# Kernel tuning notes

Hardware: AMD Instinct MI355X
Metric: run time of the kernel (lower is better)

The kernel has to match this reference:

```python
import jax, jax.numpy as jnp
import numpy as np

EMBED = 512
HEADS = 8
HEAD_DIM = EMBED // HEADS
LN_EPS = 1e-5


def setup_inputs() -> dict:
    key = jax.random.key(0)
    ks = jax.random.split(key, 13)
    B, L = 4, 2048
    s = 1.0 / np.sqrt(EMBED)
    inp = {
        "values": jax.random.normal(ks[0], (B, L, EMBED), dtype=jnp.float32),
        "keys": jax.random.normal(ks[1], (B, L, EMBED), dtype=jnp.float32),
        "query": jax.random.normal(ks[2], (B, L, EMBED), dtype=jnp.float32),
        "Wq": jax.random.uniform(ks[3], (EMBED, EMBED), jnp.float32, -s, s),
        "bq": jax.random.uniform(ks[4], (EMBED,), jnp.float32, -s, s),
        "Wk": jax.random.uniform(ks[5], (EMBED, EMBED), jnp.float32, -s, s),
        "bk": jax.random.uniform(ks[6], (EMBED,), jnp.float32, -s, s),
        "Wv": jax.random.uniform(ks[7], (EMBED, EMBED), jnp.float32, -s, s),
        "bv": jax.random.uniform(ks[8], (EMBED,), jnp.float32, -s, s),
        "Wo": jax.random.uniform(ks[9], (EMBED, EMBED), jnp.float32, -s, s),
        "bo": jax.random.uniform(ks[10], (EMBED,), jnp.float32, -s, s),
        "ln_g": jnp.ones((EMBED,), jnp.float32),
        "ln_b": jnp.zeros((EMBED,), jnp.float32),
    }
    return inp


def reference(values, keys, query, Wq, bq, Wk, bk, Wv, bv, Wo, bo, ln_g, ln_b):
    B, L, _ = query.shape
    # separate QKV linears (torch Linear: x @ W^T + b)
    Q = (query @ Wq.T + bq).reshape(B, L, HEADS, HEAD_DIM)
    K = (keys @ Wk.T + bk).reshape(B, L, HEADS, HEAD_DIM)
    V = (values @ Wv.T + bv).reshape(B, L, HEADS, HEAD_DIM)
    # explicit QK^T scores: [B, H, Q, K]
    scores = jnp.einsum("nqhd,nkhd->nhqk", Q, K) / np.sqrt(HEAD_DIM)
    attn = jax.nn.softmax(scores, axis=-1)
    out = jnp.einsum("nhqk,nkhd->nqhd", attn, V).reshape(B, L, EMBED)
    out = out @ Wo.T + bo
    # residual + LayerNorm (dropout = identity in eval)
    x = out + query
    mu = jnp.mean(x, axis=-1, keepdims=True)
    var = jnp.var(x, axis=-1, keepdims=True)
    return (x - mu) * jax.lax.rsqrt(var + LN_EPS) * ln_g + ln_b
```

## Files before the change

### kernel.cpp

```cpp
#include <hip/hip_runtime.h>

typedef short bf16x8 __attribute__((ext_vector_type(8)));
typedef short s16x4 __attribute__((ext_vector_type(4)));
typedef float f32x4 __attribute__((ext_vector_type(4)));
typedef unsigned int uint4v __attribute__((ext_vector_type(4)));
typedef unsigned int uint2v __attribute__((ext_vector_type(2)));

#define BLM   8192
#define EMB   512
#define LSEQ  2048
#define NHEAD 8
#define HDIM  64

typedef __attribute__((address_space(3))) char lds_ch;

__device__ __forceinline__ unsigned short f2bf(float x) {
    unsigned int u = __builtin_bit_cast(unsigned int, x);
    u += 0x7FFFu + ((u >> 16) & 1u);
    return (unsigned short)(u >> 16);
}

__device__ __forceinline__ unsigned int cvtpk(float lo, float hi) {
    unsigned int r;
    asm("v_cvt_pk_bf16_f32 %0, %1, %2" : "=v"(r) : "v"(lo), "v"(hi));
    return r;
}

__device__ __forceinline__ int swz(int row, int bcol) {
    return row * 128 + (bcol ^ ((row & 7) << 4));
}

#define GLL16(g, l) __builtin_amdgcn_global_load_lds( \
    (const __attribute__((address_space(1))) void*)(g), \
    (__attribute__((address_space(3))) void*)(l), 16, 0, 0)

#define TR16(dst, a, OFF) asm volatile("ds_read_b64_tr_b16 %0, %1 offset:%2" \
    : "=v"(dst) : "v"(a), "n"(OFF))

__global__ __launch_bounds__(256) void k_gemm_qkv(
    const float* __restrict__ Xq, const float* __restrict__ Xk, const float* __restrict__ Xv,
    const float* __restrict__ Wq, const float* __restrict__ Wk, const float* __restrict__ Wv,
    const float* __restrict__ bq, const float* __restrict__ bk, const float* __restrict__ bv,
    unsigned short* __restrict__ Qb, unsigned short* __restrict__ Kb, unsigned short* __restrict__ Vb)
{
    const int z = blockIdx.z;
    const float* X    = (z == 0) ? Xq : (z == 1) ? Xk : Xv;
    const float* W    = (z == 0) ? Wq : (z == 1) ? Wk : Wv;
    const float* bias = (z == 0) ? bq : (z == 1) ? bk : bv;
    unsigned short* out = (z == 0) ? Qb : (z == 1) ? Kb : Vb;
    const float osc = (z == 0) ? 0.125f * 1.44269504088896340736f : 1.0f;

    __shared__ __align__(16) char lds[32768];
    char* As = lds;
    char* Bs = lds + 16384;

    const int tid  = threadIdx.x;
    const int lane = tid & 63;
    const int wave = tid >> 6;
    const int wm = wave >> 1, wn = wave & 1;
    const int lr = lane & 15, lk = lane >> 4;
    const int m0 = blockIdx.x * 128, n0 = blockIdx.y * 128;

    f32x4 acc[4][4] = {};

    for (int kt = 0; kt < 8; ++kt) {
        const int k0 = kt * 64;
        __syncthreads();
        #pragma unroll
        for (int i = 0; i < 8; ++i) {
            int f = tid + i * 256;
            int r = f >> 4, c4 = f & 15;
            float4 v = *(const float4*)(X + (size_t)(m0 + r) * EMB + k0 + c4 * 4);
            uint2v p;
            p.x = cvtpk(v.x, v.y);
            p.y = cvtpk(v.z, v.w);
            *(uint2v*)(As + swz(r, c4 * 8)) = p;
        }
        #pragma unroll
        for (int i = 0; i < 8; ++i) {
            int f = tid + i * 256;
            int r = f >> 4, c4 = f & 15;
            float4 v = *(const float4*)(W + (size_t)(n0 + r) * EMB + k0 + c4 * 4);
            uint2v p;
            p.x = cvtpk(v.x, v.y);
            p.y = cvtpk(v.z, v.w);
            *(uint2v*)(Bs + swz(r, c4 * 8)) = p;
        }
        __syncthreads();
        #pragma unroll
        for (int ks = 0; ks < 2; ++ks) {
            bf16x8 af[4], bfr[4];
            #pragma unroll
            for (int fm = 0; fm < 4; ++fm)
                af[fm] = *(const bf16x8*)(As + swz(wm * 64 + fm * 16 + lr, ks * 64 + lk * 16));
            #pragma unroll
            for (int fn = 0; fn < 4; ++fn)
                bfr[fn] = *(const bf16x8*)(Bs + swz(wn * 64 + fn * 16 + lr, ks * 64 + lk * 16));
            #pragma unroll
            for (int fm = 0; fm < 4; ++fm)
                #pragma unroll
                for (int fn = 0; fn < 4; ++fn)
                    acc[fm][fn] = __builtin_amdgcn_mfma_f32_16x16x32_bf16(af[fm], bfr[fn], acc[fm][fn], 0, 0, 0);
        }
    }
    #pragma unroll
    for (int fn = 0; fn < 4; ++fn) {
        int n = n0 + wn * 64 + fn * 16 + lr;
        float bv_ = bias[n];
        #pragma unroll
        for (int fm = 0; fm < 4; ++fm) {
            int mb = m0 + wm * 64 + fm * 16 + lk * 4;
            #pragma unroll
            for (int j = 0; j < 4; ++j)
                out[(size_t)(mb + j) * EMB + n] = f2bf((acc[fm][fn][j] + bv_) * osc);
        }
    }
}

__global__ __launch_bounds__(256) void k_gemm_out(
    const unsigned short* __restrict__ AO, const float* __restrict__ Wo,
    const float* __restrict__ bo, const float* __restrict__ res,
    float* __restrict__ Xout)
{
    __shared__ __align__(16) char lds[32768];
    char* As = lds;
    char* Bs = lds + 16384;

    const int tid  = threadIdx.x;
    const int lane = tid & 63;
    const int wave = tid >> 6;
    const int wm = wave >> 1, wn = wave & 1;
    const int lr = lane & 15, lk = lane >> 4;
    const int m0 = blockIdx.x * 128, n0 = blockIdx.y * 128;

    f32x4 acc[4][4] = {};

    for (int kt = 0; kt < 8; ++kt) {
        const int k0 = kt * 64;
        __syncthreads();
        #pragma unroll
        for (int i = 0; i < 4; ++i) {
            int f = tid + i * 256;
            int r = f >> 3, c8 = f & 7;
            uint4v v = *(const uint4v*)(AO + (size_t)(m0 + r) * EMB + k0 + c8 * 8);
            *(uint4v*)(As + swz(r, c8 * 16)) = v;
        }
        #pragma unroll
        for (int i = 0; i < 8; ++i) {
            int f = tid + i * 256;
            int r = f >> 4, c4 = f & 15;
            float4 v = *(const float4*)(Wo + (size_t)(n0 + r) * EMB + k0 + c4 * 4);
            uint2v p;
            p.x = cvtpk(v.x, v.y);
            p.y = cvtpk(v.z, v.w);
            *(uint2v*)(Bs + swz(r, c4 * 8)) = p;
        }
        __syncthreads();
        #pragma unroll
        for (int ks = 0; ks < 2; ++ks) {
            bf16x8 af[4], bfr[4];
            #pragma unroll
            for (int fm = 0; fm < 4; ++fm)
                af[fm] = *(const bf16x8*)(As + swz(wm * 64 + fm * 16 + lr, ks * 64 + lk * 16));
            #pragma unroll
            for (int fn = 0; fn < 4; ++fn)
                bfr[fn] = *(const bf16x8*)(Bs + swz(wn * 64 + fn * 16 + lr, ks * 64 + lk * 16));
            #pragma unroll
            for (int fm = 0; fm < 4; ++fm)
                #pragma unroll
                for (int fn = 0; fn < 4; ++fn)
                    acc[fm][fn] = __builtin_amdgcn_mfma_f32_16x16x32_bf16(af[fm], bfr[fn], acc[fm][fn], 0, 0, 0);
        }
    }
    #pragma unroll
    for (int fn = 0; fn < 4; ++fn) {
        int n = n0 + wn * 64 + fn * 16 + lr;
        float bv_ = bo[n];
        #pragma unroll
        for (int fm = 0; fm < 4; ++fm) {
            int mb = m0 + wm * 64 + fm * 16 + lk * 4;
            #pragma unroll
            for (int j = 0; j < 4; ++j) {
                size_t idx = (size_t)(mb + j) * EMB + n;
                Xout[idx] = acc[fm][fn][j] + bv_ + res[idx];
            }
        }
    }
}

__global__ __launch_bounds__(512, 4) void k_attn(
    const unsigned short* __restrict__ Qb, const unsigned short* __restrict__ Kb,
    const unsigned short* __restrict__ Vb, unsigned short* __restrict__ AO)
{
    __shared__ __align__(16) char lds[65536];
    lds_ch* LB = (lds_ch*)lds;

    const int tid  = threadIdx.x;
    const int lane = tid & 63;
    const int wave = tid >> 6;
    const int lr = lane & 15, lk = lane >> 4;

    const int bh = blockIdx.y;
    const int b = bh >> 3, h = bh & 7;
    const size_t base = (size_t)b * LSEQ * EMB + h * HDIM;
    const int q0 = blockIdx.x * 128 + wave * 16;

    const int c0 = tid, c1 = tid + 512;
    auto kcol = [](int c) { int r = c >> 3; return ((c & 7) * 8) ^ ((r & 7) * 8); };
    const unsigned short* srcK0 = Kb + base + (size_t)(c0 >> 3) * EMB + kcol(c0);
    const unsigned short* srcK1 = Kb + base + (size_t)(c1 >> 3) * EMB + kcol(c1);
    auto vsrc = [&](int c) {
        int kv = ((c >> 3) & 31) * 4 + ((c >> 1) & 3);
        int d  = (c >> 8) * 16 + (c & 1) * 8;
        return Vb + base + (size_t)kv * EMB + d;
    };
    const unsigned short* srcV0 = vsrc(c0);
    const unsigned short* srcV1 = vsrc(c1);

    auto stage = [&](int par) {
        lds_ch* kd = LB + par * 16384 + wave * 1024;
        lds_ch* vd = LB + 32768 + par * 16384 + wave * 1024;
        GLL16(srcK0, kd);
        GLL16(srcK1, kd + 8192);
        GLL16(srcV0, vd);
        GLL16(srcV1, vd + 8192);
        srcK0 += 128 * EMB; srcK1 += 128 * EMB;
        srcV0 += 128 * EMB; srcV1 += 128 * EMB;
    };

    bf16x8 qf[2];
    #pragma unroll
    for (int ks = 0; ks < 2; ++ks)
        qf[ks] = *(const bf16x8*)(Qb + base + (size_t)(q0 + lr) * EMB + ks * 32 + lk * 8);

    f32x4 oaccT[4] = {};
    float lrow = 0.f;

    lds_ch* vadB = LB + 32768 + lk * 128 + lr * 2;

    stage(0);

    for (int t = 0; t < 16; ++t) {
        const int par = t & 1;
        __syncthreads();
        if (t < 15) stage(par ^ 1);

        char* Kl = lds + par * 16384;
        f32x4 sacc[8] = {};
        #pragma unroll
        for (int ks = 0; ks < 2; ++ks) {
            bf16x8 kf[8];
            #pragma unroll
            for (int blk = 0; blk < 8; ++blk)
                kf[blk] = *(const bf16x8*)(Kl + swz(blk * 16 + lr, ks * 64 + lk * 16));
            #pragma unroll
            for (int blk = 0; blk < 8; ++blk)
                sacc[blk] = __builtin_amdgcn_mfma_f32_16x16x32_bf16(kf[blk], qf[ks], sacc[blk], 0, 0, 0);
        }

        #pragma unroll
        for (int blk = 0; blk < 8; ++blk)
            #pragma unroll
            for (int j = 0; j < 4; ++j)
                sacc[blk][j] = __builtin_amdgcn_exp2f(sacc[blk][j]);
        f32x4 ps0 = sacc[0] + sacc[1];
        f32x4 ps1 = sacc[2] + sacc[3];
        f32x4 ps2 = sacc[4] + sacc[5];
        f32x4 ps3 = sacc[6] + sacc[7];
        f32x4 ps  = (ps0 + ps1) + (ps2 + ps3);
        float rs  = (ps[0] + ps[1]) + (ps[2] + ps[3]);
        rs += __shfl_xor(rs, 16);
        rs += __shfl_xor(rs, 32);
        lrow += rs;

        bf16x8 pf[4];
        #pragma unroll
        for (int k = 0; k < 4; ++k) {
            uint4v w;
            w.x = cvtpk(sacc[2 * k][0],     sacc[2 * k][1]);
            w.y = cvtpk(sacc[2 * k][2],     sacc[2 * k][3]);
            w.z = cvtpk(sacc[2 * k + 1][0], sacc[2 * k + 1][1]);
            w.w = cvtpk(sacc[2 * k + 1][2], sacc[2 * k + 1][3]);
            pf[k] = __builtin_bit_cast(bf16x8, w);
        }

        lds_ch* vad = vadB + par * 16384;
        #pragma unroll
        for (int fd = 0; fd < 4; ++fd) {
            uint2v t0, t1, t2, t3, t4, t5, t6, t7;
            TR16(t0, vad, 0);    TR16(t1, vad, 512);
            TR16(t2, vad, 1024); TR16(t3, vad, 1536);
            TR16(t4, vad, 2048); TR16(t5, vad, 2560);
            TR16(t6, vad, 3072); TR16(t7, vad, 3584);
            asm volatile("s_waitcnt lgkmcnt(0)" ::: "memory");
            __builtin_amdgcn_sched_barrier(0);
            uint4v w0; w0.x = t0.x; w0.y = t0.y; w0.z = t1.x; w0.w = t1.y;
            uint4v w1; w1.x = t2.x; w1.y = t2.y; w1.z = t3.x; w1.w = t3.y;
            uint4v w2; w2.x = t4.x; w2.y = t4.y; w2.z = t5.x; w2.w = t5.y;
            uint4v w3; w3.x = t6.x; w3.y = t6.y; w3.z = t7.x; w3.w = t7.y;
            oaccT[fd] = __builtin_amdgcn_mfma_f32_16x16x32_bf16(__builtin_bit_cast(bf16x8, w0), pf[0], oaccT[fd], 0, 0, 0);
            oaccT[fd] = __builtin_amdgcn_mfma_f32_16x16x32_bf16(__builtin_bit_cast(bf16x8, w1), pf[1], oaccT[fd], 0, 0, 0);
            oaccT[fd] = __builtin_amdgcn_mfma_f32_16x16x32_bf16(__builtin_bit_cast(bf16x8, w2), pf[2], oaccT[fd], 0, 0, 0);
            oaccT[fd] = __builtin_amdgcn_mfma_f32_16x16x32_bf16(__builtin_bit_cast(bf16x8, w3), pf[3], oaccT[fd], 0, 0, 0);
            vad += 4096;
        }
    }

    float inv = 1.f / lrow;
    unsigned short* aorow = AO + base + (size_t)(q0 + lr) * EMB;
    #pragma unroll
    for (int fd = 0; fd < 4; ++fd) {
        s16x4 s;
        #pragma unroll
        for (int j = 0; j < 4; ++j) s[j] = (short)f2bf(oaccT[fd][j] * inv);
        *(s16x4*)(aorow + fd * 16 + lk * 4) = s;
    }
}

__global__ __launch_bounds__(64) void k_ln(
    const float* __restrict__ X, const float* __restrict__ g,
    const float* __restrict__ bta, float* __restrict__ out)
{
    const int row = blockIdx.x, lane = threadIdx.x;
    const float* x = X + (size_t)row * EMB;
    float4 a = *(const float4*)(x + lane * 8);
    float4 c = *(const float4*)(x + lane * 8 + 4);
    float s  = a.x + a.y + a.z + a.w + c.x + c.y + c.z + c.w;
    float sq = a.x*a.x + a.y*a.y + a.z*a.z + a.w*a.w + c.x*c.x + c.y*c.y + c.z*c.z + c.w*c.w;
    #pragma unroll
    for (int msk = 1; msk < 64; msk <<= 1) { s += __shfl_xor(s, msk); sq += __shfl_xor(sq, msk); }
    float mu  = s * (1.f / 512.f);
    float var = sq * (1.f / 512.f) - mu * mu;
    float rs  = rsqrtf(var + 1e-5f);
    float4 g0 = *(const float4*)(g + lane * 8), g1 = *(const float4*)(g + lane * 8 + 4);
    float4 b0 = *(const float4*)(bta + lane * 8), b1 = *(const float4*)(bta + lane * 8 + 4);
    float4 o0, o1;
    o0.x = (a.x - mu) * rs * g0.x + b0.x;  o0.y = (a.y - mu) * rs * g0.y + b0.y;
    o0.z = (a.z - mu) * rs * g0.z + b0.z;  o0.w = (a.w - mu) * rs * g0.w + b0.w;
    o1.x = (c.x - mu) * rs * g1.x + b1.x;  o1.y = (c.y - mu) * rs * g1.y + b1.y;
    o1.z = (c.z - mu) * rs * g1.z + b1.z;  o1.w = (c.w - mu) * rs * g1.w + b1.w;
    *(float4*)(out + (size_t)row * EMB + lane * 8) = o0;
    *(float4*)(out + (size_t)row * EMB + lane * 8 + 4) = o1;
}

extern "C" void kernel_launch(void* const* d_in, const int* in_sizes, int n_in,
                              void* d_out, int out_size, void* d_ws, size_t ws_size,
                              hipStream_t stream) {
    const float* values = (const float*)d_in[0];
    const float* keys   = (const float*)d_in[1];
    const float* query  = (const float*)d_in[2];
    const float* Wq = (const float*)d_in[3];  const float* bq = (const float*)d_in[4];
    const float* Wk = (const float*)d_in[5];  const float* bk = (const float*)d_in[6];
    const float* Wv = (const float*)d_in[7];  const float* bv = (const float*)d_in[8];
    const float* Wo = (const float*)d_in[9];  const float* bo = (const float*)d_in[10];
    const float* lng = (const float*)d_in[11];
    const float* lnb = (const float*)d_in[12];

    char* ws = (char*)d_ws;
    unsigned short* Qb = (unsigned short*)(ws);
    unsigned short* Kb = (unsigned short*)(ws + 8u  * 1024 * 1024);
    unsigned short* Vb = (unsigned short*)(ws + 16u * 1024 * 1024);
    unsigned short* AO = (unsigned short*)(ws + 24u * 1024 * 1024);
    float*          Xr = (float*)(ws);

    dim3 gqkv(64, 4, 3);
    k_gemm_qkv<<<gqkv, 256, 0, stream>>>(query, keys, values, Wq, Wk, Wv, bq, bk, bv, Qb, Kb, Vb);
    k_attn<<<dim3(16, 32), 512, 0, stream>>>(Qb, Kb, Vb, AO);
    k_gemm_out<<<dim3(64, 4), 256, 0, stream>>>(AO, Wo, bo, query, Xr);
    k_ln<<<8192, 64, 0, stream>>>(Xr, lng, lnb, (float*)d_out);
}
```

Measured before the change: 100.3 us.

## Register-prefetch GEMM tiles, add MFMA priority, defer softmax row-sum reduction

Both projection GEMMs now load the next K-tile from global memory into registers while the current tile is consumed, so global latency overlaps with MFMA work. Launch bounds are raised to request three blocks per CU. In the attention loop, s_setprio raises wave priority around the MFMA sections, and the per-row sum shuffle reduction moves out of the loop into a single reduction after it. The prefetch registers add pressure, which could conflict with the occupancy target or cause spills.

```diff
diff --git a/kernel.cpp b/kernel.cpp
--- a/kernel.cpp
+++ b/kernel.cpp
@@ -37,7 +37,7 @@
 #define TR16(dst, a, OFF) asm volatile("ds_read_b64_tr_b16 %0, %1 offset:%2" \
     : "=v"(dst) : "v"(a), "n"(OFF))
 
-__global__ __launch_bounds__(256) void k_gemm_qkv(
+__global__ __launch_bounds__(256, 3) void k_gemm_qkv(
     const float* __restrict__ Xq, const float* __restrict__ Xk, const float* __restrict__ Xv,
     const float* __restrict__ Wq, const float* __restrict__ Wk, const float* __restrict__ Wv,
     const float* __restrict__ bq, const float* __restrict__ bk, const float* __restrict__ bv,
@@ -63,28 +63,35 @@
 
     f32x4 acc[4][4] = {};
 
+    const float* pa = X + (size_t)(m0 + (tid >> 4)) * EMB + (tid & 15) * 4;
+    const float* pb = W + (size_t)(n0 + (tid >> 4)) * EMB + (tid & 15) * 4;
+
+    float4 ar[8], br[8];
+    #pragma unroll
+    for (int i = 0; i < 8; ++i) {
+        ar[i] = *(const float4*)(pa + (size_t)i * 16 * EMB);
+        br[i] = *(const float4*)(pb + (size_t)i * 16 * EMB);
+    }
+    pa += 64; pb += 64;
+
     for (int kt = 0; kt < 8; ++kt) {
-        const int k0 = kt * 64;
         __syncthreads();
         #pragma unroll
         for (int i = 0; i < 8; ++i) {
             int f = tid + i * 256;
             int r = f >> 4, c4 = f & 15;
-            float4 v = *(const float4*)(X + (size_t)(m0 + r) * EMB + k0 + c4 * 4);
-            uint2v p;
-            p.x = cvtpk(v.x, v.y);
-            p.y = cvtpk(v.z, v.w);
+            uint2v p; p.x = cvtpk(ar[i].x, ar[i].y); p.y = cvtpk(ar[i].z, ar[i].w);
             *(uint2v*)(As + swz(r, c4 * 8)) = p;
-        }
-        #pragma unroll
-        for (int i = 0; i < 8; ++i) {
-            int f = tid + i * 256;
-            int r = f >> 4, c4 = f & 15;
-            float4 v = *(const float4*)(W + (size_t)(n0 + r) * EMB + k0 + c4 * 4);
-            uint2v p;
-            p.x = cvtpk(v.x, v.y);
-            p.y = cvtpk(v.z, v.w);
-            *(uint2v*)(Bs + swz(r, c4 * 8)) = p;
+            uint2v q; q.x = cvtpk(br[i].x, br[i].y); q.y = cvtpk(br[i].z, br[i].w);
+            *(uint2v*)(Bs + swz(r, c4 * 8)) = q;
+        }
+        if (kt < 7) {
+            #pragma unroll
+            for (int i = 0; i < 8; ++i) {
+                ar[i] = *(const float4*)(pa + (size_t)i * 16 * EMB);
+                br[i] = *(const float4*)(pb + (size_t)i * 16 * EMB);
+            }
+            pa += 64; pb += 64;
         }
         __syncthreads();
         #pragma unroll
@@ -117,7 +124,7 @@
     }
 }
 
-__global__ __launch_bounds__(256) void k_gemm_out(
+__global__ __launch_bounds__(256, 3) void k_gemm_out(
     const unsigned short* __restrict__ AO, const float* __restrict__ Wo,
     const float* __restrict__ bo, const float* __restrict__ res,
     float* __restrict__ Xout)
@@ -135,25 +142,37 @@
 
     f32x4 acc[4][4] = {};
 
+    const unsigned short* pA = AO + (size_t)(m0 + (tid >> 3)) * EMB + (tid & 7) * 8;
+    const float* pB = Wo + (size_t)(n0 + (tid >> 4)) * EMB + (tid & 15) * 4;
+
+    uint4v arA[4]; float4 brB[8];
+    #pragma unroll
+    for (int i = 0; i < 4; ++i) arA[i] = *(const uint4v*)(pA + (size_t)i * 32 * EMB);
+    #pragma unroll
+    for (int i = 0; i < 8; ++i) brB[i] = *(const float4*)(pB + (size_t)i * 16 * EMB);
+    pA += 64; pB += 64;
+
     for (int kt = 0; kt < 8; ++kt) {
-        const int k0 = kt * 64;
         __syncthreads();
         #pragma unroll
         for (int i = 0; i < 4; ++i) {
             int f = tid + i * 256;
             int r = f >> 3, c8 = f & 7;
-            uint4v v = *(const uint4v*)(AO + (size_t)(m0 + r) * EMB + k0 + c8 * 8);
-            *(uint4v*)(As + swz(r, c8 * 16)) = v;
+            *(uint4v*)(As + swz(r, c8 * 16)) = arA[i];
         }
         #pragma unroll
         for (int i = 0; i < 8; ++i) {
             int f = tid + i * 256;
             int r = f >> 4, c4 = f & 15;
-            float4 v = *(const float4*)(Wo + (size_t)(n0 + r) * EMB + k0 + c4 * 4);
-            uint2v p;
-            p.x = cvtpk(v.x, v.y);
-            p.y = cvtpk(v.z, v.w);
-            *(uint2v*)(Bs + swz(r, c4 * 8)) = p;
+            uint2v q; q.x = cvtpk(brB[i].x, brB[i].y); q.y = cvtpk(brB[i].z, brB[i].w);
+            *(uint2v*)(Bs + swz(r, c4 * 8)) = q;
+        }
+        if (kt < 7) {
+            #pragma unroll
+            for (int i = 0; i < 4; ++i) arA[i] = *(const uint4v*)(pA + (size_t)i * 32 * EMB);
+            #pragma unroll
+            for (int i = 0; i < 8; ++i) brB[i] = *(const float4*)(pB + (size_t)i * 16 * EMB);
+            pA += 64; pB += 64;
         }
         __syncthreads();
         #pragma unroll
@@ -247,6 +266,7 @@
 
         char* Kl = lds + par * 16384;
         f32x4 sacc[8] = {};
+        __builtin_amdgcn_s_setprio(1);
         #pragma unroll
         for (int ks = 0; ks < 2; ++ks) {
             bf16x8 kf[8];
@@ -257,6 +277,7 @@
             for (int blk = 0; blk < 8; ++blk)
                 sacc[blk] = __builtin_amdgcn_mfma_f32_16x16x32_bf16(kf[blk], qf[ks], sacc[blk], 0, 0, 0);
         }
+        __builtin_amdgcn_s_setprio(0);
 
         #pragma unroll
         for (int blk = 0; blk < 8; ++blk)
@@ -268,10 +289,7 @@
         f32x4 ps2 = sacc[4] + sacc[5];
         f32x4 ps3 = sacc[6] + sacc[7];
         f32x4 ps  = (ps0 + ps1) + (ps2 + ps3);
-        float rs  = (ps[0] + ps[1]) + (ps[2] + ps[3]);
-        rs += __shfl_xor(rs, 16);
-        rs += __shfl_xor(rs, 32);
-        lrow += rs;
+        lrow += (ps[0] + ps[1]) + (ps[2] + ps[3]);
 
         bf16x8 pf[4];
         #pragma unroll
@@ -285,6 +303,7 @@
         }
 
         lds_ch* vad = vadB + par * 16384;
+        __builtin_amdgcn_s_setprio(1);
         #pragma unroll
         for (int fd = 0; fd < 4; ++fd) {
             uint2v t0, t1, t2, t3, t4, t5, t6, t7;
@@ -304,8 +323,11 @@
             oaccT[fd] = __builtin_amdgcn_mfma_f32_16x16x32_bf16(__builtin_bit_cast(bf16x8, w3), pf[3], oaccT[fd], 0, 0, 0);
             vad += 4096;
         }
-    }
-
+        __builtin_amdgcn_s_setprio(0);
+    }
+
+    lrow += __shfl_xor(lrow, 16);
+    lrow += __shfl_xor(lrow, 32);
     float inv = 1.f / lrow;
     unsigned short* aorow = AO + base + (size_t)(q0 + lr) * EMB;
     #pragma unroll
```

Result: faster. 90.95 us (-9.4%).
